# Kernel optimization log

Measured on AMD Instinct MI355X. Metric: run time of the kernel, lower is better.

## Reference

```python
import jax, jax.numpy as jnp
import numpy as np

MX_D, MN_D, CENTERS, WIDTH, SLOPE = 10.0, 0.0, 16, 1.0, 0.01
T_STEPS = 3


def _lrelu(x):
    return jax.nn.leaky_relu(x, SLOPE)


def _gauss(d):
    # d: [B,E,1] distances -> [B,E,CENTERS] gaussian radial basis
    mu = jnp.linspace(MN_D, MX_D, CENTERS, dtype=d.dtype)
    return jnp.exp(-jnp.square((d - mu[None, None, :]) / WIDTH))


def _equiv_message(v, idx2, n_recv, W1, W2, b, aw, ab):
    # v: [B,E,F] = concat(sender feats, receiver feats, bond feats).
    # Outer-product expand over receiver-cell axis (einsum with one-hot),
    # permutation-equivariant linear (local term + cell-sum term), LeakyReLU,
    # gather receiver cell, sigmoid attention gate, scatter_add to receivers.
    B, E, _ = v.shape
    O = W1.shape[1]
    oh = jax.nn.one_hot(idx2, n_recv, dtype=v.dtype)                 # [E,N]
    y_loc = jnp.einsum('bef,fo->beo', v, W1)                          # per-cell term
    y_sum = jnp.einsum('bef,fo->beo', v, W2) + b                      # cell-sum term (sum_n v*oh = v)
    y = _lrelu(y_loc[..., None] * oh[None, :, None, :] + y_sum[..., None])  # [B,E,O,N]
    gidx = jnp.broadcast_to(idx2[None, :, None, None], (B, E, O, 1))
    lat = jnp.take_along_axis(y, gidx, axis=3)[..., 0]                # [B,E,O]
    lat = jax.nn.sigmoid(lat @ aw + ab[None, None, :]) * lat          # attention gating
    return jnp.zeros((B, n_recv, O), v.dtype).at[:, idx2].add(lat)    # scatter_add over receivers


def _forward(sites, bonds, sites_p, bonds_sp, bonds_ps,
             se_W, se_b, sep_W, sep_b, ee_W, ee_b, eep_W, eep_b,
             eq_W1_ss, eq_W2_ss, eq_b_ss, att_w_ss, att_b_ss,
             eq_W1_ps, eq_W2_ps, eq_b_ps, att_w_ps, att_b_ps,
             eq_W1_sp, eq_W2_sp, eq_b_sp, att_w_sp, att_b_sp,
             nu_W1, nu_b1, nu_W2, nu_b2, nup_W1, nup_b1, nup_W2, nup_b2,
             p1_W, p1_b, p2a_W, p2a_b, p2b_W, p2b_b, p3_W, p3_b,
             idx1, idx2, idx1_sp, idx2_sp, idx1_ps, idx2_ps):
    s = _lrelu(sites @ se_W + se_b)          # [B,N,D] site embedding
    sp = _lrelu(sites_p @ sep_W + sep_b)     # [B,Np,D] pore embedding
    be = _lrelu(_gauss(bonds) @ ee_W + ee_b)
    bsp = _lrelu(_gauss(bonds_sp) @ eep_W + eep_b)
    bps = _lrelu(_gauss(bonds_ps) @ eep_W + eep_b)
    N, Np = s.shape[1], sp.shape[1]
    for t in range(T_STEPS):  # fixed number of message-passing layers
        v_ss = jnp.concatenate([s[:, idx1], s[:, idx2], be], -1)
        m = _equiv_message(v_ss, idx2, N, eq_W1_ss[t], eq_W2_ss[t], eq_b_ss[t], att_w_ss[t], att_b_ss[t])
        v_ps = jnp.concatenate([sp[:, idx1_ps], s[:, idx2_ps], bps], -1)
        m_ps = _equiv_message(v_ps, idx2_ps, N, eq_W1_ps[t], eq_W2_ps[t], eq_b_ps[t], att_w_ps[t], att_b_ps[t])
        v_sp = jnp.concatenate([s[:, idx1_sp], sp[:, idx2_sp], bsp], -1)
        m_sp = _equiv_message(v_sp, idx2_sp, Np, eq_W1_sp[t], eq_W2_sp[t], eq_b_sp[t], att_w_sp[t], att_b_sp[t])
        h = jnp.concatenate([s, m, m_ps], -1)
        h = _lrelu(_lrelu(h @ nu_W1[t] + nu_b1[t]) @ nu_W2[t] + nu_b2[t])
        s = s + h                              # residual node update (sites)
        hp = jnp.concatenate([sp, m_sp], -1)
        hp = _lrelu(_lrelu(hp @ nup_W1[t] + nup_b1[t]) @ nup_W2[t] + nup_b2[t])
        sp = sp + hp                           # residual node update (pores)
    x = _lrelu(s @ p1_W + p1_b).sum(1)        # sum pool over sites
    x = _lrelu(x @ p2a_W + p2a_b)
    x = _lrelu(x @ p2b_W + p2b_b)
    return x @ p3_W + p3_b                    # [B, out_size]


def setup_inputs():
    key = jax.random.key(0)
    ks = iter(jax.random.split(key, 80))
    B, N, Np, E, Esp = 4, 128, 16, 1280, 1024
    D, C, O, M, T = 32, CENTERS, 32, 64, T_STEPS
    Fin = 2 * D + 16  # sender + receiver + edge embedding

    def nrm(shape, fan):
        return jax.random.normal(next(ks), shape, jnp.float32) / np.float32(np.sqrt(fan))

    inp = {}
    inp['sites'] = jax.random.uniform(next(ks), (B, N, 1), jnp.float32)
    inp['bonds'] = jax.random.uniform(next(ks), (B, E, 1), jnp.float32) * MX_D
    inp['sites_p'] = jax.random.uniform(next(ks), (B, Np, 2), jnp.float32)
    inp['bonds_sp'] = jax.random.uniform(next(ks), (B, Esp, 1), jnp.float32) * MX_D
    inp['bonds_ps'] = jax.random.uniform(next(ks), (B, Esp, 1), jnp.float32) * MX_D
    inp['idx1'] = jax.random.randint(next(ks), (E,), 0, N, jnp.int32)
    inp['idx2'] = jax.random.randint(next(ks), (E,), 0, N, jnp.int32)
    inp['idx1_sp'] = jax.random.randint(next(ks), (Esp,), 0, N, jnp.int32)
    inp['idx2_sp'] = jax.random.randint(next(ks), (Esp,), 0, Np, jnp.int32)
    inp['idx1_ps'] = jax.random.randint(next(ks), (Esp,), 0, Np, jnp.int32)
    inp['idx2_ps'] = jax.random.randint(next(ks), (Esp,), 0, N, jnp.int32)
    # embeddings
    inp['se_W'] = nrm((1, D), 1); inp['se_b'] = nrm((D,), D)
    inp['sep_W'] = nrm((2, D), 2); inp['sep_b'] = nrm((D,), D)
    inp['ee_W'] = nrm((C, 16), C); inp['ee_b'] = nrm((16,), 16)
    inp['eep_W'] = nrm((C, 16), C); inp['eep_b'] = nrm((16,), 16)
    # equivariant message layers (stacked over T steps)
    for suf in ('ss', 'ps', 'sp'):
        inp['eq_W1_' + suf] = nrm((T, Fin, O), Fin)
        inp['eq_W2_' + suf] = nrm((T, Fin, O), Fin)
        inp['eq_b_' + suf] = nrm((T, O), O)
        inp['att_w_' + suf] = nrm((T, O, 1), O)
        inp['att_b_' + suf] = nrm((T, 1), 1)
    # node updates: sites take 2 message streams, pores take 1
    inp['nu_W1'] = nrm((T, D + 2 * O, D), D + 2 * O); inp['nu_b1'] = nrm((T, D), D)
    inp['nu_W2'] = nrm((T, D, D), D); inp['nu_b2'] = nrm((T, D), D)
    inp['nup_W1'] = nrm((T, D + O, D), D + O); inp['nup_b1'] = nrm((T, D), D)
    inp['nup_W2'] = nrm((T, D, D), D); inp['nup_b2'] = nrm((T, D), D)
    # prediction head
    inp['p1_W'] = nrm((D, M), D); inp['p1_b'] = nrm((M,), M)
    inp['p2a_W'] = nrm((M, M), M); inp['p2a_b'] = nrm((M,), M)
    inp['p2b_W'] = nrm((M, M), M); inp['p2b_b'] = nrm((M,), M)
    inp['p3_W'] = nrm((M, 1), M); inp['p3_b'] = nrm((1,), 1)
    return inp


def reference(sites, bonds, sites_p, bonds_sp, bonds_ps,
              se_W, se_b, sep_W, sep_b, ee_W, ee_b, eep_W, eep_b,
              eq_W1_ss, eq_W2_ss, eq_b_ss, att_w_ss, att_b_ss,
              eq_W1_ps, eq_W2_ps, eq_b_ps, att_w_ps, att_b_ps,
              eq_W1_sp, eq_W2_sp, eq_b_sp, att_w_sp, att_b_sp,
              nu_W1, nu_b1, nu_W2, nu_b2, nup_W1, nup_b1, nup_W2, nup_b2,
              p1_W, p1_b, p2a_W, p2a_b, p2b_W, p2b_b, p3_W, p3_b,
              idx1, idx2, idx1_sp, idx2_sp, idx1_ps, idx2_ps):
    return _forward(sites, bonds, sites_p, bonds_sp, bonds_ps,
                    se_W, se_b, sep_W, sep_b, ee_W, ee_b, eep_W, eep_b,
                    eq_W1_ss, eq_W2_ss, eq_b_ss, att_w_ss, att_b_ss,
                    eq_W1_ps, eq_W2_ps, eq_b_ps, att_w_ps, att_b_ps,
                    eq_W1_sp, eq_W2_sp, eq_b_sp, att_w_sp, att_b_sp,
                    nu_W1, nu_b1, nu_W2, nu_b2, nup_W1, nup_b1, nup_W2, nup_b2,
                    p1_W, p1_b, p2a_W, p2a_b, p2b_W, p2b_b, p3_W, p3_b,
                    idx1, idx2, idx1_sp, idx2_sp, idx1_ps, idx2_ps)
```

## Files before the change

kernel.cpp:

```cpp
#include <hip/hip_runtime.h>
#include <math.h>

#define BB   4
#define NN   128
#define NPP  16
#define EEE  1280
#define ESP  1024
#define DD   32
#define CC   16
#define OO   32
#define FIN  80
#define MMM  64
#define TT   3
#define TPB  256

constexpr int OFF_S    = 0;
constexpr int OFF_SP   = OFF_S    + BB*NN*DD;
constexpr int OFF_BE   = OFF_SP   + BB*NPP*DD;
constexpr int OFF_BSP  = OFF_BE   + BB*EEE*CC;
constexpr int OFF_BPS  = OFF_BSP  + BB*ESP*CC;
constexpr int OFF_MSS  = OFF_BPS  + BB*ESP*CC;
constexpr int OFF_MPS  = OFF_MSS  + TT*BB*NN*OO;
constexpr int OFF_MSP  = OFF_MPS  + TT*BB*NN*OO;
constexpr int OFF_MEND = OFF_MSP  + TT*BB*NPP*OO;
constexpr int ZM       = OFF_MEND - OFF_MSS;
constexpr int OFF_SASS = OFF_MEND;
constexpr int OFF_SBSS = OFF_SASS + BB*NN*OO;
constexpr int OFF_SBPS = OFF_SBSS + BB*NN*OO;
constexpr int OFF_SASP = OFF_SBPS + BB*NN*OO;
constexpr int OFF_PAPS = OFF_SASP + BB*NN*OO;
constexpr int OFF_PBSP = OFF_PAPS + BB*NPP*OO;
constexpr int WS_TOTAL = OFF_PBSP + BB*NPP*OO;

__device__ __forceinline__ float lrelu(float x) { return x > 0.f ? x : 0.01f * x; }

__device__ __forceinline__ void edge_embed(float d, const float* W, const float* bvec, float* out) {
    float g[CC];
#pragma unroll
    for (int c = 0; c < CC; ++c) {
        float mu = (10.0f / 15.0f) * (float)c;
        float z = d - mu;
        g[c] = expf(-z * z);
    }
#pragma unroll
    for (int j = 0; j < CC; ++j) {
        float a = bvec[j];
#pragma unroll
        for (int c = 0; c < CC; ++c) a += g[c] * W[c * CC + j];
        out[j] = lrelu(a);
    }
}

__global__ __launch_bounds__(TPB) void k_init(
    const float* sites, const float* bonds, const float* sites_p,
    const float* bonds_sp, const float* bonds_ps,
    const float* se_W, const float* se_b, const float* sep_W, const float* sep_b,
    const float* ee_W, const float* ee_b, const float* eep_W, const float* eep_b,
    const float* eqW1_ss, const float* eqW2_ss,
    const float* eqW1_ps, const float* eqW2_ps,
    const float* eqW1_sp, const float* eqW2_sp,
    float* ws)
{
    __shared__ float smem[4416];
    const int blk = blockIdx.x;
    const int tid = threadIdx.x;

    {
        const int totalA = ZM + BB*EEE + BB*ESP + BB*ESP;
        for (int i = blk*TPB + tid; i < totalA; i += gridDim.x*TPB) {
            int r = i;
            if (r < ZM) { ws[OFF_MSS + r] = 0.f; continue; }
            r -= ZM;
            if (r < BB*EEE) { edge_embed(bonds[r],    ee_W,  ee_b,  ws + OFF_BE  + r*CC); continue; }
            r -= BB*EEE;
            if (r < BB*ESP) { edge_embed(bonds_sp[r], eep_W, eep_b, ws + OFF_BSP + r*CC); continue; }
            r -= BB*ESP;
            edge_embed(bonds_ps[r], eep_W, eep_b, ws + OFF_BPS + r*CC);
        }
    }
    if (blk < 72) {
        const int el = tid >> 5, o = tid & 31;
        float* sP   = smem;
        float* sRow = smem + 4160;
        if (blk < 64) {
            const int g = blk*8 + el;
            float x = sites[g];
            float v0 = lrelu(x * se_W[o] + se_b[o]);
            ws[OFF_S + g*DD + o] = v0;
            sRow[el*32 + o] = v0;
            for (int i2 = tid; i2 < 4096; i2 += TPB) {
                int m = i2 >> 10, j = i2 & 1023, d = j >> 5, oo = j & 31;
                int row = (m == 1 || m == 2) ? (32 + d) : d;
                float wv;
                if (m < 2)      wv = eqW1_ss[row*OO + oo] + eqW2_ss[row*OO + oo];
                else if (m==2)  wv = eqW1_ps[row*OO + oo] + eqW2_ps[row*OO + oo];
                else            wv = eqW1_sp[row*OO + oo] + eqW2_sp[row*OO + oo];
                sP[i2] = wv;
            }
            __syncthreads();
            float p0=0.f,p1=0.f,p2=0.f,p3=0.f;
#pragma unroll
            for (int d = 0; d < 32; ++d) {
                float sv = sRow[el*32 + d];
                p0 += sv * sP[        d*32 + o];
                p1 += sv * sP[1024 +  d*32 + o];
                p2 += sv * sP[2048 +  d*32 + o];
                p3 += sv * sP[3072 +  d*32 + o];
            }
            ws[OFF_SASS + g*OO + o] = p0;
            ws[OFF_SBSS + g*OO + o] = p1;
            ws[OFF_SBPS + g*OO + o] = p2;
            ws[OFF_SASP + g*OO + o] = p3;
        } else {
            const int g = (blk-64)*8 + el;
            float x0 = sites_p[g*2], x1 = sites_p[g*2+1];
            float v0 = lrelu(x0 * sep_W[o] + x1 * sep_W[DD + o] + sep_b[o]);
            ws[OFF_SP + g*DD + o] = v0;
            sRow[el*32 + o] = v0;
            for (int i2 = tid; i2 < 2048; i2 += TPB) {
                int m = i2 >> 10, j = i2 & 1023, d = j >> 5, oo = j & 31;
                int row = (m == 0) ? d : (32 + d);
                float wv;
                if (m == 0) wv = eqW1_ps[row*OO + oo] + eqW2_ps[row*OO + oo];
                else        wv = eqW1_sp[row*OO + oo] + eqW2_sp[row*OO + oo];
                sP[i2] = wv;
            }
            __syncthreads();
            float p0=0.f,p1=0.f;
#pragma unroll
            for (int d = 0; d < 32; ++d) {
                float sv = sRow[el*32 + d];
                p0 += sv * sP[        d*32 + o];
                p1 += sv * sP[1024 +  d*32 + o];
            }
            ws[OFF_PAPS + g*OO + o] = p0;
            ws[OFF_PBSP + g*OO + o] = p1;
        }
    }
}

__global__ __launch_bounds__(TPB) void k_edges(
    const float* eqW1_ss, const float* eqW2_ss, const float* eqb_ss, const float* aw_ss, const float* ab_ss,
    const float* eqW1_ps, const float* eqW2_ps, const float* eqb_ps, const float* aw_ps, const float* ab_ps,
    const float* eqW1_sp, const float* eqW2_sp, const float* eqb_sp, const float* aw_sp, const float* ab_sp,
    const int* idx1, const int* idx2, const int* idx1_sp, const int* idx2_sp,
    const int* idx1_ps, const int* idx2_ps,
    float* ws, int t)
{
    __shared__ float sWe[CC*OO];
    __shared__ float sB[OO], sAw[OO];
    __shared__ float sAb;

    const int tid = threadIdx.x;
    const int blk = blockIdx.x;
    const int el = tid >> 5, o = tid & 31;

    constexpr int NB_SS = BB*EEE/8;
    constexpr int NB_PS = BB*ESP/8;

    const float *w1p, *w2p, *bp, *awp, *abp;
    const float *SAb, *SBb, *ef; float* mb;
    int s1, s2;

    if (blk < NB_SS) {
        const int rloc = blk*8 + el;
        const int b = rloc / EEE, e = rloc - b*EEE;
        s1 = idx1[e]; s2 = idx2[e];
        SAb = ws + OFF_SASS + b*(NN*OO);
        SBb = ws + OFF_SBSS + b*(NN*OO);
        ef  = ws + OFF_BE  + rloc*CC;
        mb  = ws + OFF_MSS + t*(BB*NN*OO) + b*(NN*OO);
        w1p = eqW1_ss; w2p = eqW2_ss; bp = eqb_ss; awp = aw_ss; abp = ab_ss;
    } else if (blk < NB_SS + NB_PS) {
        const int rloc = (blk - NB_SS)*8 + el;
        const int b = rloc >> 10, e = rloc & (ESP-1);
        s1 = idx1_ps[e]; s2 = idx2_ps[e];
        SAb = ws + OFF_PAPS + b*(NPP*OO);
        SBb = ws + OFF_SBPS + b*(NN*OO);
        ef  = ws + OFF_BPS + rloc*CC;
        mb  = ws + OFF_MPS + t*(BB*NN*OO) + b*(NN*OO);
        w1p = eqW1_ps; w2p = eqW2_ps; bp = eqb_ps; awp = aw_ps; abp = ab_ps;
    } else {
        const int rloc = (blk - NB_SS - NB_PS)*8 + el;
        const int b = rloc >> 10, e = rloc & (ESP-1);
        s1 = idx1_sp[e]; s2 = idx2_sp[e];
        SAb = ws + OFF_SASP + b*(NN*OO);
        SBb = ws + OFF_PBSP + b*(NPP*OO);
        ef  = ws + OFF_BSP + rloc*CC;
        mb  = ws + OFF_MSP + t*(BB*NPP*OO) + b*(NPP*OO);
        w1p = eqW1_sp; w2p = eqW2_sp; bp = eqb_sp; awp = aw_sp; abp = ab_sp;
    }

    const float* wa = w1p + t*(FIN*OO) + 2*DD*OO;
    const float* wb = w2p + t*(FIN*OO) + 2*DD*OO;
    for (int i = tid; i < CC*OO; i += TPB) sWe[i] = wa[i] + wb[i];
    if (tid < OO) { sB[tid] = bp[t*OO + tid]; sAw[tid] = awp[t*OO + tid]; }
    if (tid == 0) sAb = abp[t];
    __syncthreads();

    const float4 e0 = *(const float4*)(ef);
    const float4 e1 = *(const float4*)(ef + 4);
    const float4 e2 = *(const float4*)(ef + 8);
    const float4 e3 = *(const float4*)(ef + 12);

    float acc = sB[o] + SAb[s1*OO + o] + SBb[s2*OO + o];
    acc += e0.x*sWe[ 0*32+o] + e0.y*sWe[ 1*32+o] + e0.z*sWe[ 2*32+o] + e0.w*sWe[ 3*32+o];
    acc += e1.x*sWe[ 4*32+o] + e1.y*sWe[ 5*32+o] + e1.z*sWe[ 6*32+o] + e1.w*sWe[ 7*32+o];
    acc += e2.x*sWe[ 8*32+o] + e2.y*sWe[ 9*32+o] + e2.z*sWe[10*32+o] + e2.w*sWe[11*32+o];
    acc += e3.x*sWe[12*32+o] + e3.y*sWe[13*32+o] + e3.z*sWe[14*32+o] + e3.w*sWe[15*32+o];

    float u = lrelu(acc);
    float r = u * sAw[o];
#pragma unroll
    for (int mm = 16; mm > 0; mm >>= 1) r += __shfl_xor(r, mm, 32);
    float gate = 1.f / (1.f + expf(-(r + sAb)));
    atomicAdd(&mb[s2*OO + o], gate * u);
}

__global__ __launch_bounds__(TPB) void k_nodes(
    const float* nuW1, const float* nub1, const float* nuW2, const float* nub2,
    const float* nupW1, const float* nupb1, const float* nupW2, const float* nupb2,
    const float* eqW1_ss, const float* eqW2_ss,
    const float* eqW1_ps, const float* eqW2_ps,
    const float* eqW1_sp, const float* eqW2_sp,
    float* ws, int t)
{
    __shared__ float smem[5184];
    const int tid = threadIdx.x;
    const int blk = blockIdx.x;
    float* sW1 = smem;
    float* sW2 = smem + 3072;
    float* sb1 = smem + 4096;
    float* sb2 = smem + 4128;
    float* sh  = smem + 4160;
    float* su  = smem + 4928;
    const float* mss = ws + OFF_MSS + t*(BB*NN*OO);
    const float* mps = ws + OFF_MPS + t*(BB*NN*OO);
    const float* msp = ws + OFF_MSP + t*(BB*NPP*OO);
    const int el = tid >> 5, o = tid & 31;

    if (blk < 64) {
        const float* W1 = nuW1 + t*96*32;
        const float* W2 = nuW2 + t*32*32;
        for (int i = tid; i < 96*32; i += TPB) sW1[i] = W1[i];
        for (int i = tid; i < 32*32; i += TPB) sW2[i] = W2[i];
        if (tid < 32) { sb1[tid] = nub1[t*32 + tid]; sb2[tid] = nub2[t*32 + tid]; }
        for (int i = tid; i < 8*96; i += TPB) {
            int e2 = i / 96, f = i - e2*96;
            int g = blk*8 + e2;
            float v;
            if (f < 32)      v = ws[OFF_S + g*DD + f];
            else if (f < 64) v = mss[g*OO + (f-32)];
            else             v = mps[g*OO + (f-64)];
            sh[i] = v;
        }
        __syncthreads();
        float acc = sb1[o];
#pragma unroll
        for (int f = 0; f < 96; ++f) acc += sh[el*96 + f] * sW1[f*32 + o];
        su[el*32 + o] = lrelu(acc);
        __syncthreads();
        float acc2 = sb2[o];
#pragma unroll
        for (int k = 0; k < 32; ++k) acc2 += su[el*32 + k] * sW2[k*32 + o];
        const int g = blk*8 + el;
        float snew = sh[el*96 + o] + lrelu(acc2);
        __syncthreads();
        ws[OFF_S + g*DD + o] = snew;
        float* sRow = smem + 4928;
        sRow[el*32 + o] = snew;
        if (t < TT-1) {
            const int tn = t + 1;
            float* sP = smem;
            for (int i2 = tid; i2 < 4096; i2 += TPB) {
                int m = i2 >> 10, j = i2 & 1023, d = j >> 5, oo = j & 31;
                int row = (m == 1 || m == 2) ? (32 + d) : d;
                float wv;
                if (m < 2)     wv = eqW1_ss[tn*FIN*OO + row*OO + oo] + eqW2_ss[tn*FIN*OO + row*OO + oo];
                else if (m==2) wv = eqW1_ps[tn*FIN*OO + row*OO + oo] + eqW2_ps[tn*FIN*OO + row*OO + oo];
                else           wv = eqW1_sp[tn*FIN*OO + row*OO + oo] + eqW2_sp[tn*FIN*OO + row*OO + oo];
                sP[i2] = wv;
            }
            __syncthreads();
            float p0=0.f,p1=0.f,p2=0.f,p3=0.f;
#pragma unroll
            for (int d = 0; d < 32; ++d) {
                float sv = sRow[el*32 + d];
                p0 += sv * sP[        d*32 + o];
                p1 += sv * sP[1024 +  d*32 + o];
                p2 += sv * sP[2048 +  d*32 + o];
                p3 += sv * sP[3072 +  d*32 + o];
            }
            ws[OFF_SASS + g*OO + o] = p0;
            ws[OFF_SBSS + g*OO + o] = p1;
            ws[OFF_SBPS + g*OO + o] = p2;
            ws[OFF_SASP + g*OO + o] = p3;
        }
    } else {
        const int u2 = blk - 64;
        const float* W1 = nupW1 + t*64*32;
        const float* W2 = nupW2 + t*32*32;
        for (int i = tid; i < 64*32; i += TPB) sW1[i] = W1[i];
        for (int i = tid; i < 32*32; i += TPB) sW2[i] = W2[i];
        if (tid < 32) { sb1[tid] = nupb1[t*32 + tid]; sb2[tid] = nupb2[t*32 + tid]; }
        for (int i = tid; i < 8*64; i += TPB) {
            int e2 = i >> 6, f = i & 63;
            int g = u2*8 + e2;
            float v;
            if (f < 32) v = ws[OFF_SP + g*DD + f];
            else        v = msp[g*OO + (f-32)];
            sh[i] = v;
        }
        __syncthreads();
        float acc = sb1[o];
#pragma unroll
        for (int f = 0; f < 64; ++f) acc += sh[el*64 + f] * sW1[f*32 + o];
        su[el*32 + o] = lrelu(acc);
        __syncthreads();
        float acc2 = sb2[o];
#pragma unroll
        for (int k = 0; k < 32; ++k) acc2 += su[el*32 + k] * sW2[k*32 + o];
        const int g = u2*8 + el;
        float snew = sh[el*64 + o] + lrelu(acc2);
        __syncthreads();
        ws[OFF_SP + g*DD + o] = snew;
        float* sRow = smem + 4928;
        sRow[el*32 + o] = snew;
        if (t < TT-1) {
            const int tn = t + 1;
            float* sP = smem;
            for (int i2 = tid; i2 < 2048; i2 += TPB) {
                int m = i2 >> 10, j = i2 & 1023, d = j >> 5, oo = j & 31;
                int row = (m == 0) ? d : (32 + d);
                float wv;
                if (m == 0) wv = eqW1_ps[tn*FIN*OO + row*OO + oo] + eqW2_ps[tn*FIN*OO + row*OO + oo];
                else        wv = eqW1_sp[tn*FIN*OO + row*OO + oo] + eqW2_sp[tn*FIN*OO + row*OO + oo];
                sP[i2] = wv;
            }
            __syncthreads();
            float p0=0.f,p1=0.f;
#pragma unroll
            for (int d = 0; d < 32; ++d) {
                float sv = sRow[el*32 + d];
                p0 += sv * sP[        d*32 + o];
                p1 += sv * sP[1024 +  d*32 + o];
            }
            ws[OFF_PAPS + g*OO + o] = p0;
            ws[OFF_PBSP + g*OO + o] = p1;
        }
    }
}

__global__ __launch_bounds__(TPB) void k_head(
    const float* p1W, const float* p1b, const float* p2aW, const float* p2ab,
    const float* p2bW, const float* p2bb, const float* p3W, const float* p3b,
    const float* ws, float* out)
{
    __shared__ float sS[NN * DD];
    __shared__ float sW[DD * MMM];
    __shared__ float part[4][MMM];
    __shared__ float xv[MMM], yv[MMM], zv[MMM];

    const int b = blockIdx.x;
    const int tid = threadIdx.x;
    const float* s = ws + OFF_S + b * NN * DD;

    for (int i = tid; i < NN * DD; i += TPB) sS[i] = s[i];
    for (int i = tid; i < DD * MMM; i += TPB) sW[i] = p1W[i];
    __syncthreads();

    const int m = tid & 63;
    const int q = tid >> 6;
    float accp = 0.f;
    for (int n = q * 32; n < q * 32 + 32; ++n) {
        float a = p1b[m];
#pragma unroll
        for (int d = 0; d < DD; ++d) a += sS[n * DD + d] * sW[d * MMM + m];
        accp += lrelu(a);
    }
    part[q][m] = accp;
    __syncthreads();

    if (tid < MMM) xv[tid] = part[0][tid] + part[1][tid] + part[2][tid] + part[3][tid];
    __syncthreads();
    if (tid < MMM) {
        float a = p2ab[tid];
#pragma unroll
        for (int k = 0; k < MMM; ++k) a += xv[k] * p2aW[k * MMM + tid];
        yv[tid] = lrelu(a);
    }
    __syncthreads();
    if (tid < MMM) {
        float a = p2bb[tid];
#pragma unroll
        for (int k = 0; k < MMM; ++k) a += yv[k] * p2bW[k * MMM + tid];
        zv[tid] = lrelu(a);
    }
    __syncthreads();
    if (tid == 0) {
        float a = p3b[0];
#pragma unroll
        for (int k = 0; k < MMM; ++k) a += zv[k] * p3W[k];
        out[b] = a;
    }
}

extern "C" void kernel_launch(void* const* d_in, const int* in_sizes, int n_in,
                              void* d_out, int out_size, void* d_ws, size_t ws_size,
                              hipStream_t stream) {
    (void)in_sizes; (void)n_in; (void)out_size; (void)ws_size;
    const float* sites    = (const float*)d_in[0];
    const float* bonds    = (const float*)d_in[1];
    const float* sites_p  = (const float*)d_in[2];
    const float* bonds_sp = (const float*)d_in[3];
    const float* bonds_ps = (const float*)d_in[4];
    const int* idx1    = (const int*)d_in[5];
    const int* idx2    = (const int*)d_in[6];
    const int* idx1_sp = (const int*)d_in[7];
    const int* idx2_sp = (const int*)d_in[8];
    const int* idx1_ps = (const int*)d_in[9];
    const int* idx2_ps = (const int*)d_in[10];
    const float* se_W  = (const float*)d_in[11];
    const float* se_b  = (const float*)d_in[12];
    const float* sep_W = (const float*)d_in[13];
    const float* sep_b = (const float*)d_in[14];
    const float* ee_W  = (const float*)d_in[15];
    const float* ee_b  = (const float*)d_in[16];
    const float* eep_W = (const float*)d_in[17];
    const float* eep_b = (const float*)d_in[18];
    const float* eqW1_ss = (const float*)d_in[19];
    const float* eqW2_ss = (const float*)d_in[20];
    const float* eqb_ss  = (const float*)d_in[21];
    const float* aw_ss   = (const float*)d_in[22];
    const float* ab_ss   = (const float*)d_in[23];
    const float* eqW1_ps = (const float*)d_in[24];
    const float* eqW2_ps = (const float*)d_in[25];
    const float* eqb_ps  = (const float*)d_in[26];
    const float* aw_ps   = (const float*)d_in[27];
    const float* ab_ps   = (const float*)d_in[28];
    const float* eqW1_sp = (const float*)d_in[29];
    const float* eqW2_sp = (const float*)d_in[30];
    const float* eqb_sp  = (const float*)d_in[31];
    const float* aw_sp   = (const float*)d_in[32];
    const float* ab_sp   = (const float*)d_in[33];
    const float* nuW1  = (const float*)d_in[34];
    const float* nub1  = (const float*)d_in[35];
    const float* nuW2  = (const float*)d_in[36];
    const float* nub2  = (const float*)d_in[37];
    const float* nupW1 = (const float*)d_in[38];
    const float* nupb1 = (const float*)d_in[39];
    const float* nupW2 = (const float*)d_in[40];
    const float* nupb2 = (const float*)d_in[41];
    const float* p1W  = (const float*)d_in[42];
    const float* p1b  = (const float*)d_in[43];
    const float* p2aW = (const float*)d_in[44];
    const float* p2ab = (const float*)d_in[45];
    const float* p2bW = (const float*)d_in[46];
    const float* p2bb = (const float*)d_in[47];
    const float* p3W  = (const float*)d_in[48];
    const float* p3b  = (const float*)d_in[49];

    float* ws  = (float*)d_ws;
    float* out = (float*)d_out;

    k_init<<<256, TPB, 0, stream>>>(sites, bonds, sites_p, bonds_sp, bonds_ps,
                                    se_W, se_b, sep_W, sep_b, ee_W, ee_b, eep_W, eep_b,
                                    eqW1_ss, eqW2_ss, eqW1_ps, eqW2_ps, eqW1_sp, eqW2_sp, ws);

    const int edge_blocks = BB*EEE/8 + BB*ESP/8 + BB*ESP/8;
    for (int t = 0; t < TT; ++t) {
        k_edges<<<edge_blocks, TPB, 0, stream>>>(
            eqW1_ss, eqW2_ss, eqb_ss, aw_ss, ab_ss,
            eqW1_ps, eqW2_ps, eqb_ps, aw_ps, ab_ps,
            eqW1_sp, eqW2_sp, eqb_sp, aw_sp, ab_sp,
            idx1, idx2, idx1_sp, idx2_sp, idx1_ps, idx2_ps, ws, t);
        k_nodes<<<72, TPB, 0, stream>>>(nuW1, nub1, nuW2, nub2,
                                        nupW1, nupb1, nupW2, nupb2,
                                        eqW1_ss, eqW2_ss, eqW1_ps, eqW2_ps, eqW1_sp, eqW2_sp,
                                        ws, t);
    }
    k_head<<<4, TPB, 0, stream>>>(p1W, p1b, p2aW, p2ab, p2bW, p2bb, p3W, p3b, ws, out);
}
```

Measured before the change: 59.99 us.

## Fuse edge and node kernels via receiver CSR gather instead of atomics

Builds CSR lists of edges per receiver in the init kernel, then replaces the separate edge-scatter and node-update kernels with one per-step kernel. Each block gathers its receivers' incoming edges, reduces messages in shared memory, runs the node MLP and writes next-step projections. Projections are double-buffered so a single launch per step can read the old ones and write the new ones. The head's first layer pooling is folded in via atomics. This removes the atomic scatter and halves the launches per step, at the cost of serial CSR construction and less parallelism for high in-degree nodes.

Measured after the change: 196.1 us. 3.27x slower.

```diff
diff --git a/kernel.cpp b/kernel.cpp
--- a/kernel.cpp
+++ b/kernel.cpp
@@ -15,24 +15,45 @@
 #define TPB  256
 
 constexpr int OFF_S    = 0;
-constexpr int OFF_SP   = OFF_S    + BB*NN*DD;
-constexpr int OFF_BE   = OFF_SP   + BB*NPP*DD;
-constexpr int OFF_BSP  = OFF_BE   + BB*EEE*CC;
-constexpr int OFF_BPS  = OFF_BSP  + BB*ESP*CC;
-constexpr int OFF_MSS  = OFF_BPS  + BB*ESP*CC;
-constexpr int OFF_MPS  = OFF_MSS  + TT*BB*NN*OO;
-constexpr int OFF_MSP  = OFF_MPS  + TT*BB*NN*OO;
-constexpr int OFF_MEND = OFF_MSP  + TT*BB*NPP*OO;
-constexpr int ZM       = OFF_MEND - OFF_MSS;
-constexpr int OFF_SASS = OFF_MEND;
-constexpr int OFF_SBSS = OFF_SASS + BB*NN*OO;
-constexpr int OFF_SBPS = OFF_SBSS + BB*NN*OO;
-constexpr int OFF_SASP = OFF_SBPS + BB*NN*OO;
-constexpr int OFF_PAPS = OFF_SASP + BB*NN*OO;
-constexpr int OFF_PBSP = OFF_PAPS + BB*NPP*OO;
-constexpr int WS_TOTAL = OFF_PBSP + BB*NPP*OO;
+constexpr int OFF_SP   = OFF_S   + BB*NN*DD;
+constexpr int OFF_BE   = OFF_SP  + BB*NPP*DD;
+constexpr int OFF_BSP  = OFF_BE  + BB*EEE*CC;
+constexpr int OFF_BPS  = OFF_BSP + BB*ESP*CC;
+constexpr int OFF_PRJ  = OFF_BPS + BB*ESP*CC;
+constexpr int P_SASS = 0;
+constexpr int P_SBSS = P_SASS + BB*NN*OO;
+constexpr int P_SBPS = P_SBSS + BB*NN*OO;
+constexpr int P_SASP = P_SBPS + BB*NN*OO;
+constexpr int P_PAPS = P_SASP + BB*NN*OO;
+constexpr int P_PBSP = P_PAPS + BB*NPP*OO;
+constexpr int PRJ_SZ = P_PBSP + BB*NPP*OO;
+constexpr int OFF_POOL = OFF_PRJ + 2*PRJ_SZ;
+constexpr int OFF_CSR  = OFF_POOL + BB*MMM;
+constexpr int SS_PTR  = 0;
+constexpr int SS_LIST = SS_PTR + NN + 1;
+constexpr int PS_PTR  = SS_LIST + EEE;
+constexpr int PS_LIST = PS_PTR + NN + 1;
+constexpr int SP_PTR  = PS_LIST + ESP;
+constexpr int SP_LIST = SP_PTR + NPP + 1;
 
 __device__ __forceinline__ float lrelu(float x) { return x > 0.f ? x : 0.01f * x; }
+
+__device__ __forceinline__ float dot16(const float* ef, const float* sWe, int o) {
+    float4 f0 = *(const float4*)(ef);
+    float4 f1 = *(const float4*)(ef + 4);
+    float4 f2 = *(const float4*)(ef + 8);
+    float4 f3 = *(const float4*)(ef + 12);
+    return f0.x*sWe[ 0*32+o] + f0.y*sWe[ 1*32+o] + f0.z*sWe[ 2*32+o] + f0.w*sWe[ 3*32+o]
+         + f1.x*sWe[ 4*32+o] + f1.y*sWe[ 5*32+o] + f1.z*sWe[ 6*32+o] + f1.w*sWe[ 7*32+o]
+         + f2.x*sWe[ 8*32+o] + f2.y*sWe[ 9*32+o] + f2.z*sWe[10*32+o] + f2.w*sWe[11*32+o]
+         + f3.x*sWe[12*32+o] + f3.y*sWe[13*32+o] + f3.z*sWe[14*32+o] + f3.w*sWe[15*32+o];
+}
+
+__device__ __forceinline__ float red32(float r) {
+#pragma unroll
+    for (int mm = 16; mm > 0; mm >>= 1) r += __shfl_xor(r, mm, 32);
+    return r;
+}
 
 __device__ __forceinline__ void edge_embed(float d, const float* W, const float* bvec, float* out) {
     float g[CC];
@@ -51,9 +72,30 @@
     }
 }
 
+__device__ void csr_build(const int* recv, int E, int R, int* ptr, int* list, int* scnt) {
+    const int tid = threadIdx.x;
+    if (tid < R) {
+        int c = 0;
+        for (int e = 0; e < E; ++e) c += (recv[e] == tid) ? 1 : 0;
+        scnt[tid] = c;
+    }
+    __syncthreads();
+    if (tid == 0) {
+        int run = 0;
+        for (int i = 0; i < R; ++i) { int c = scnt[i]; scnt[i] = run; ptr[i] = run; run += c; }
+        ptr[R] = run;
+    }
+    __syncthreads();
+    if (tid < R) {
+        int pos = scnt[tid];
+        for (int e = 0; e < E; ++e) if (recv[e] == tid) list[pos++] = e;
+    }
+}
+
 __global__ __launch_bounds__(TPB) void k_init(
     const float* sites, const float* bonds, const float* sites_p,
     const float* bonds_sp, const float* bonds_ps,
+    const int* idx2, const int* idx2_ps, const int* idx2_sp,
     const float* se_W, const float* se_b, const float* sep_W, const float* sep_b,
     const float* ee_W, const float* ee_b, const float* eep_W, const float* eep_b,
     const float* eqW1_ss, const float* eqW2_ss,
@@ -66,11 +108,11 @@
     const int tid = threadIdx.x;
 
     {
-        const int totalA = ZM + BB*EEE + BB*ESP + BB*ESP;
+        const int totalA = BB*MMM + BB*EEE + BB*ESP + BB*ESP;
         for (int i = blk*TPB + tid; i < totalA; i += gridDim.x*TPB) {
             int r = i;
-            if (r < ZM) { ws[OFF_MSS + r] = 0.f; continue; }
-            r -= ZM;
+            if (r < BB*MMM) { ws[OFF_POOL + r] = 0.f; continue; }
+            r -= BB*MMM;
             if (r < BB*EEE) { edge_embed(bonds[r],    ee_W,  ee_b,  ws + OFF_BE  + r*CC); continue; }
             r -= BB*EEE;
             if (r < BB*ESP) { edge_embed(bonds_sp[r], eep_W, eep_b, ws + OFF_BSP + r*CC); continue; }
@@ -79,6 +121,7 @@
         }
     }
     if (blk < 72) {
+        float* prj0 = ws + OFF_PRJ;
         const int el = tid >> 5, o = tid & 31;
         float* sP   = smem;
         float* sRow = smem + 4160;
@@ -90,7 +133,7 @@
             sRow[el*32 + o] = v0;
             for (int i2 = tid; i2 < 4096; i2 += TPB) {
                 int m = i2 >> 10, j = i2 & 1023, d = j >> 5, oo = j & 31;
-                int row = (m == 1 || m == 2) ? (32 + d) : d;
+                int row = (m == 1 || m == 2) ? (DD + d) : d;
                 float wv;
                 if (m < 2)      wv = eqW1_ss[row*OO + oo] + eqW2_ss[row*OO + oo];
                 else if (m==2)  wv = eqW1_ps[row*OO + oo] + eqW2_ps[row*OO + oo];
@@ -107,10 +150,10 @@
                 p2 += sv * sP[2048 +  d*32 + o];
                 p3 += sv * sP[3072 +  d*32 + o];
             }
-            ws[OFF_SASS + g*OO + o] = p0;
-            ws[OFF_SBSS + g*OO + o] = p1;
-            ws[OFF_SBPS + g*OO + o] = p2;
-            ws[OFF_SASP + g*OO + o] = p3;
+            prj0[P_SASS + g*OO + o] = p0;
+            prj0[P_SBSS + g*OO + o] = p1;
+            prj0[P_SBPS + g*OO + o] = p2;
+            prj0[P_SASP + g*OO + o] = p3;
         } else {
             const int g = (blk-64)*8 + el;
             float x0 = sites_p[g*2], x1 = sites_p[g*2+1];
@@ -119,7 +162,7 @@
             sRow[el*32 + o] = v0;
             for (int i2 = tid; i2 < 2048; i2 += TPB) {
                 int m = i2 >> 10, j = i2 & 1023, d = j >> 5, oo = j & 31;
-                int row = (m == 0) ? d : (32 + d);
+                int row = (m == 0) ? d : (DD + d);
                 float wv;
                 if (m == 0) wv = eqW1_ps[row*OO + oo] + eqW2_ps[row*OO + oo];
                 else        wv = eqW1_sp[row*OO + oo] + eqW2_sp[row*OO + oo];
@@ -133,275 +176,214 @@
                 p0 += sv * sP[        d*32 + o];
                 p1 += sv * sP[1024 +  d*32 + o];
             }
-            ws[OFF_PAPS + g*OO + o] = p0;
-            ws[OFF_PBSP + g*OO + o] = p1;
-        }
-    }
-}
-
-__global__ __launch_bounds__(TPB) void k_edges(
+            prj0[P_PAPS + g*OO + o] = p0;
+            prj0[P_PBSP + g*OO + o] = p1;
+        }
+    }
+    if (blk >= 253) {
+        int* csr  = (int*)(ws + OFF_CSR);
+        int* scnt = (int*)smem;
+        if (blk == 255)      csr_build(idx2,    EEE, NN,  csr + SS_PTR, csr + SS_LIST, scnt);
+        else if (blk == 254) csr_build(idx2_ps, ESP, NN,  csr + PS_PTR, csr + PS_LIST, scnt);
+        else                 csr_build(idx2_sp, ESP, NPP, csr + SP_PTR, csr + SP_LIST, scnt);
+    }
+}
+
+__global__ __launch_bounds__(TPB) void k_step(
     const float* eqW1_ss, const float* eqW2_ss, const float* eqb_ss, const float* aw_ss, const float* ab_ss,
     const float* eqW1_ps, const float* eqW2_ps, const float* eqb_ps, const float* aw_ps, const float* ab_ps,
     const float* eqW1_sp, const float* eqW2_sp, const float* eqb_sp, const float* aw_sp, const float* ab_sp,
-    const int* idx1, const int* idx2, const int* idx1_sp, const int* idx2_sp,
-    const int* idx1_ps, const int* idx2_ps,
+    const int* idx1, const int* idx1_ps, const int* idx1_sp,
+    const float* nuW1, const float* nub1, const float* nuW2, const float* nub2,
+    const float* nupW1, const float* nupb1, const float* nupW2, const float* nupb2,
+    const float* p1W, const float* p1b,
     float* ws, int t)
 {
-    __shared__ float sWe[CC*OO];
-    __shared__ float sB[OO], sAw[OO];
-    __shared__ float sAb;
-
-    const int tid = threadIdx.x;
-    const int blk = blockIdx.x;
-    const int el = tid >> 5, o = tid & 31;
-
-    constexpr int NB_SS = BB*EEE/8;
-    constexpr int NB_PS = BB*ESP/8;
-
-    const float *w1p, *w2p, *bp, *awp, *abp;
-    const float *SAb, *SBb, *ef; float* mb;
-    int s1, s2;
-
-    if (blk < NB_SS) {
-        const int rloc = blk*8 + el;
-        const int b = rloc / EEE, e = rloc - b*EEE;
-        s1 = idx1[e]; s2 = idx2[e];
-        SAb = ws + OFF_SASS + b*(NN*OO);
-        SBb = ws + OFF_SBSS + b*(NN*OO);
-        ef  = ws + OFF_BE  + rloc*CC;
-        mb  = ws + OFF_MSS + t*(BB*NN*OO) + b*(NN*OO);
-        w1p = eqW1_ss; w2p = eqW2_ss; bp = eqb_ss; awp = aw_ss; abp = ab_ss;
-    } else if (blk < NB_SS + NB_PS) {
-        const int rloc = (blk - NB_SS)*8 + el;
-        const int b = rloc >> 10, e = rloc & (ESP-1);
-        s1 = idx1_ps[e]; s2 = idx2_ps[e];
-        SAb = ws + OFF_PAPS + b*(NPP*OO);
-        SBb = ws + OFF_SBPS + b*(NN*OO);
-        ef  = ws + OFF_BPS + rloc*CC;
-        mb  = ws + OFF_MPS + t*(BB*NN*OO) + b*(NN*OO);
-        w1p = eqW1_ps; w2p = eqW2_ps; bp = eqb_ps; awp = aw_ps; abp = ab_ps;
-    } else {
-        const int rloc = (blk - NB_SS - NB_PS)*8 + el;
-        const int b = rloc >> 10, e = rloc & (ESP-1);
-        s1 = idx1_sp[e]; s2 = idx2_sp[e];
-        SAb = ws + OFF_SASP + b*(NN*OO);
-        SBb = ws + OFF_PBSP + b*(NPP*OO);
-        ef  = ws + OFF_BSP + rloc*CC;
-        mb  = ws + OFF_MSP + t*(BB*NPP*OO) + b*(NPP*OO);
-        w1p = eqW1_sp; w2p = eqW2_sp; bp = eqb_sp; awp = aw_sp; abp = ab_sp;
-    }
-
-    const float* wa = w1p + t*(FIN*OO) + 2*DD*OO;
-    const float* wb = w2p + t*(FIN*OO) + 2*DD*OO;
-    for (int i = tid; i < CC*OO; i += TPB) sWe[i] = wa[i] + wb[i];
-    if (tid < OO) { sB[tid] = bp[t*OO + tid]; sAw[tid] = awp[t*OO + tid]; }
-    if (tid == 0) sAb = abp[t];
-    __syncthreads();
-
-    const float4 e0 = *(const float4*)(ef);
-    const float4 e1 = *(const float4*)(ef + 4);
-    const float4 e2 = *(const float4*)(ef + 8);
-    const float4 e3 = *(const float4*)(ef + 12);
-
-    float acc = sB[o] + SAb[s1*OO + o] + SBb[s2*OO + o];
-    acc += e0.x*sWe[ 0*32+o] + e0.y*sWe[ 1*32+o] + e0.z*sWe[ 2*32+o] + e0.w*sWe[ 3*32+o];
-    acc += e1.x*sWe[ 4*32+o] + e1.y*sWe[ 5*32+o] + e1.z*sWe[ 6*32+o] + e1.w*sWe[ 7*32+o];
-    acc += e2.x*sWe[ 8*32+o] + e2.y*sWe[ 9*32+o] + e2.z*sWe[10*32+o] + e2.w*sWe[11*32+o];
-    acc += e3.x*sWe[12*32+o] + e3.y*sWe[13*32+o] + e3.z*sWe[14*32+o] + e3.w*sWe[15*32+o];
-
-    float u = lrelu(acc);
-    float r = u * sAw[o];
-#pragma unroll
-    for (int mm = 16; mm > 0; mm >>= 1) r += __shfl_xor(r, mm, 32);
-    float gate = 1.f / (1.f + expf(-(r + sAb)));
-    atomicAdd(&mb[s2*OO + o], gate * u);
-}
-
-__global__ __launch_bounds__(TPB) void k_nodes(
-    const float* nuW1, const float* nub1, const float* nuW2, const float* nub2,
-    const float* nupW1, const float* nupb1, const float* nupW2, const float* nupb2,
-    const float* eqW1_ss, const float* eqW2_ss,
-    const float* eqW1_ps, const float* eqW2_ps,
-    const float* eqW1_sp, const float* eqW2_sp,
-    float* ws, int t)
-{
-    __shared__ float smem[5184];
-    const int tid = threadIdx.x;
-    const int blk = blockIdx.x;
-    float* sW1 = smem;
-    float* sW2 = smem + 3072;
-    float* sb1 = smem + 4096;
-    float* sb2 = smem + 4128;
-    float* sh  = smem + 4160;
-    float* su  = smem + 4928;
-    const float* mss = ws + OFF_MSS + t*(BB*NN*OO);
-    const float* mps = ws + OFF_MPS + t*(BB*NN*OO);
-    const float* msp = ws + OFF_MSP + t*(BB*NPP*OO);
-    const int el = tid >> 5, o = tid & 31;
-
-    if (blk < 64) {
-        const float* W1 = nuW1 + t*96*32;
-        const float* W2 = nuW2 + t*32*32;
-        for (int i = tid; i < 96*32; i += TPB) sW1[i] = W1[i];
-        for (int i = tid; i < 32*32; i += TPB) sW2[i] = W2[i];
-        if (tid < 32) { sb1[tid] = nub1[t*32 + tid]; sb2[tid] = nub2[t*32 + tid]; }
-        for (int i = tid; i < 8*96; i += TPB) {
-            int e2 = i / 96, f = i - e2*96;
-            int g = blk*8 + e2;
-            float v;
-            if (f < 32)      v = ws[OFF_S + g*DD + f];
-            else if (f < 64) v = mss[g*OO + (f-32)];
-            else             v = mps[g*OO + (f-64)];
-            sh[i] = v;
-        }
-        __syncthreads();
-        float acc = sb1[o];
-#pragma unroll
-        for (int f = 0; f < 96; ++f) acc += sh[el*96 + f] * sW1[f*32 + o];
-        su[el*32 + o] = lrelu(acc);
-        __syncthreads();
-        float acc2 = sb2[o];
-#pragma unroll
-        for (int k = 0; k < 32; ++k) acc2 += su[el*32 + k] * sW2[k*32 + o];
-        const int g = blk*8 + el;
-        float snew = sh[el*96 + o] + lrelu(acc2);
-        __syncthreads();
-        ws[OFF_S + g*DD + o] = snew;
-        float* sRow = smem + 4928;
-        sRow[el*32 + o] = snew;
+    __shared__ float sWe1[512], sWe2[512], sRed[512], sH[192], sU[64], sSnew[64];
+    const int tid = threadIdx.x, blk = blockIdx.x;
+    const int slot = tid >> 5, o = tid & 31;
+    const int par = t & 1;
+    const float* PRJ  = ws + OFF_PRJ + par * PRJ_SZ;
+    float*       PRJn = ws + OFF_PRJ + (par ^ 1) * PRJ_SZ;
+    const int* csr = (const int*)(ws + OFF_CSR);
+
+    if (blk < 256) {
+        const int r = slot >> 2, q = slot & 3;
+        for (int i = tid; i < 512; i += TPB) {
+            sWe1[i] = eqW1_ss[t*FIN*OO + 2*DD*OO + i] + eqW2_ss[t*FIN*OO + 2*DD*OO + i];
+            sWe2[i] = eqW1_ps[t*FIN*OO + 2*DD*OO + i] + eqW2_ps[t*FIN*OO + 2*DD*OO + i];
+        }
+        __syncthreads();
+        const int g = blk*2 + r, b = g >> 7, n = g & 127;
+        const float bias_ss = eqb_ss[t*OO+o], awo_ss = aw_ss[t*OO+o], abs_ss = ab_ss[t];
+        const float bias_ps = eqb_ps[t*OO+o], awo_ps = aw_ps[t*OO+o], abs_ps = ab_ps[t];
+        const float sb_ss = PRJ[P_SBSS + g*OO + o];
+        const float sb_ps = PRJ[P_SBPS + g*OO + o];
+        const float* SAss = PRJ + P_SASS + b*(NN*OO);
+        const float* PAps = PRJ + P_PAPS + b*(NPP*OO);
+        const float* BEb  = ws + OFF_BE  + b*(EEE*CC);
+        const float* BPSb = ws + OFF_BPS + b*(ESP*CC);
+        float acc_ss = 0.f, acc_ps = 0.f;
+        {
+            const int e0 = csr[SS_PTR + n], e1 = csr[SS_PTR + n + 1];
+            for (int k = e0 + q; k < e1; k += 4) {
+                const int e = csr[SS_LIST + k];
+                const int s1 = idx1[e];
+                float a = bias_ss + sb_ss + SAss[s1*OO + o] + dot16(BEb + e*CC, sWe1, o);
+                float u = lrelu(a);
+                float rr = red32(u * awo_ss);
+                acc_ss += u / (1.f + expf(-(rr + abs_ss)));
+            }
+        }
+        {
+            const int e0 = csr[PS_PTR + n], e1 = csr[PS_PTR + n + 1];
+            for (int k = e0 + q; k < e1; k += 4) {
+                const int e = csr[PS_LIST + k];
+                const int s1 = idx1_ps[e];
+                float a = bias_ps + sb_ps + PAps[s1*OO + o] + dot16(BPSb + e*CC, sWe2, o);
+                float u = lrelu(a);
+                float rr = red32(u * awo_ps);
+                acc_ps += u / (1.f + expf(-(rr + abs_ps)));
+            }
+        }
+        sRed[slot*64 + o]      = acc_ss;
+        sRed[slot*64 + 32 + o] = acc_ps;
+        if (tid < 64) sH[(tid>>5)*96 + (tid&31)] = ws[OFF_S + (blk*2 + (tid>>5))*DD + (tid&31)];
+        __syncthreads();
+        if (tid < 128) {
+            const int r2 = tid >> 6, c = tid & 63;
+            sH[r2*96 + 32 + c] = sRed[(r2*4  )*64 + c] + sRed[(r2*4+1)*64 + c]
+                               + sRed[(r2*4+2)*64 + c] + sRed[(r2*4+3)*64 + c];
+        }
+        __syncthreads();
+        if (tid < 64) {
+            const int r2 = tid >> 5, oo = tid & 31;
+            const float* W1 = nuW1 + t*(96*32);
+            float a = nub1[t*32 + oo];
+#pragma unroll
+            for (int f = 0; f < 96; ++f) a += sH[r2*96 + f] * W1[f*32 + oo];
+            sU[r2*32 + oo] = lrelu(a);
+        }
+        __syncthreads();
+        if (tid < 64) {
+            const int r2 = tid >> 5, oo = tid & 31;
+            const float* W2 = nuW2 + t*(32*32);
+            float a = nub2[t*32 + oo];
+#pragma unroll
+            for (int k2 = 0; k2 < 32; ++k2) a += sU[r2*32 + k2] * W2[k2*32 + oo];
+            const float snew = sH[r2*96 + oo] + lrelu(a);
+            ws[OFF_S + (blk*2 + r2)*DD + oo] = snew;
+            sSnew[r2*32 + oo] = snew;
+        }
+        __syncthreads();
         if (t < TT-1) {
             const int tn = t + 1;
-            float* sP = smem;
-            for (int i2 = tid; i2 < 4096; i2 += TPB) {
-                int m = i2 >> 10, j = i2 & 1023, d = j >> 5, oo = j & 31;
-                int row = (m == 1 || m == 2) ? (32 + d) : d;
-                float wv;
-                if (m < 2)     wv = eqW1_ss[tn*FIN*OO + row*OO + oo] + eqW2_ss[tn*FIN*OO + row*OO + oo];
-                else if (m==2) wv = eqW1_ps[tn*FIN*OO + row*OO + oo] + eqW2_ps[tn*FIN*OO + row*OO + oo];
-                else           wv = eqW1_sp[tn*FIN*OO + row*OO + oo] + eqW2_sp[tn*FIN*OO + row*OO + oo];
-                sP[i2] = wv;
-            }
-            __syncthreads();
-            float p0=0.f,p1=0.f,p2=0.f,p3=0.f;
-#pragma unroll
-            for (int d = 0; d < 32; ++d) {
-                float sv = sRow[el*32 + d];
-                p0 += sv * sP[        d*32 + o];
-                p1 += sv * sP[1024 +  d*32 + o];
-                p2 += sv * sP[2048 +  d*32 + o];
-                p3 += sv * sP[3072 +  d*32 + o];
-            }
-            ws[OFF_SASS + g*OO + o] = p0;
-            ws[OFF_SBSS + g*OO + o] = p1;
-            ws[OFF_SBPS + g*OO + o] = p2;
-            ws[OFF_SASP + g*OO + o] = p3;
+            const int r2 = slot >> 2, m = slot & 3;
+            const int g2 = blk*2 + r2;
+            const float *w1m, *w2m; float* dst;
+            if (m == 0)      { w1m = eqW1_ss + tn*FIN*OO;         w2m = eqW2_ss + tn*FIN*OO;         dst = PRJn + P_SASS; }
+            else if (m == 1) { w1m = eqW1_ss + tn*FIN*OO + DD*OO; w2m = eqW2_ss + tn*FIN*OO + DD*OO; dst = PRJn + P_SBSS; }
+            else if (m == 2) { w1m = eqW1_ps + tn*FIN*OO + DD*OO; w2m = eqW2_ps + tn*FIN*OO + DD*OO; dst = PRJn + P_SBPS; }
+            else             { w1m = eqW1_sp + tn*FIN*OO;         w2m = eqW2_sp + tn*FIN*OO;         dst = PRJn + P_SASP; }
+            float a = 0.f;
+#pragma unroll
+            for (int d = 0; d < 32; ++d) a += sSnew[r2*32 + d] * (w1m[d*OO + o] + w2m[d*OO + o]);
+            dst[g2*OO + o] = a;
+        } else if (tid < 128) {
+            const int r2 = tid >> 6, mm = tid & 63;
+            const int g2 = blk*2 + r2, b2 = g2 >> 7;
+            float a = p1b[mm];
+#pragma unroll
+            for (int d = 0; d < 32; ++d) a += sSnew[r2*32 + d] * p1W[d*MMM + mm];
+            atomicAdd(&ws[OFF_POOL + b2*MMM + mm], lrelu(a));
         }
     } else {
-        const int u2 = blk - 64;
-        const float* W1 = nupW1 + t*64*32;
-        const float* W2 = nupW2 + t*32*32;
-        for (int i = tid; i < 64*32; i += TPB) sW1[i] = W1[i];
-        for (int i = tid; i < 32*32; i += TPB) sW2[i] = W2[i];
-        if (tid < 32) { sb1[tid] = nupb1[t*32 + tid]; sb2[tid] = nupb2[t*32 + tid]; }
-        for (int i = tid; i < 8*64; i += TPB) {
-            int e2 = i >> 6, f = i & 63;
-            int g = u2*8 + e2;
-            float v;
-            if (f < 32) v = ws[OFF_SP + g*DD + f];
-            else        v = msp[g*OO + (f-32)];
-            sh[i] = v;
-        }
-        __syncthreads();
-        float acc = sb1[o];
-#pragma unroll
-        for (int f = 0; f < 64; ++f) acc += sh[el*64 + f] * sW1[f*32 + o];
-        su[el*32 + o] = lrelu(acc);
-        __syncthreads();
-        float acc2 = sb2[o];
-#pragma unroll
-        for (int k = 0; k < 32; ++k) acc2 += su[el*32 + k] * sW2[k*32 + o];
-        const int g = u2*8 + el;
-        float snew = sh[el*64 + o] + lrelu(acc2);
-        __syncthreads();
-        ws[OFF_SP + g*DD + o] = snew;
-        float* sRow = smem + 4928;
-        sRow[el*32 + o] = snew;
-        if (t < TT-1) {
+        for (int i = tid; i < 512; i += TPB)
+            sWe1[i] = eqW1_sp[t*FIN*OO + 2*DD*OO + i] + eqW2_sp[t*FIN*OO + 2*DD*OO + i];
+        __syncthreads();
+        const int g = blk - 256, b = g >> 4, p = g & 15;
+        const float bias_sp = eqb_sp[t*OO+o], awo_sp = aw_sp[t*OO+o], abs_sp = ab_sp[t];
+        const float sb_sp = PRJ[P_PBSP + g*OO + o];
+        const float* SAsp = PRJ + P_SASP + b*(NN*OO);
+        const float* BSPb = ws + OFF_BSP + b*(ESP*CC);
+        float acc_sp = 0.f;
+        {
+            const int e0 = csr[SP_PTR + p], e1 = csr[SP_PTR + p + 1];
+            for (int k = e0 + slot; k < e1; k += 8) {
+                const int e = csr[SP_LIST + k];
+                const int s1 = idx1_sp[e];
+                float a = bias_sp + sb_sp + SAsp[s1*OO + o] + dot16(BSPb + e*CC, sWe1, o);
+                float u = lrelu(a);
+                float rr = red32(u * awo_sp);
+                acc_sp += u / (1.f + expf(-(rr + abs_sp)));
+            }
+        }
+        sRed[slot*32 + o] = acc_sp;
+        if (tid < 32) sH[tid] = ws[OFF_SP + g*DD + tid];
+        __syncthreads();
+        if (tid < 32) {
+            float mv = 0.f;
+#pragma unroll
+            for (int s2 = 0; s2 < 8; ++s2) mv += sRed[s2*32 + tid];
+            sH[32 + tid] = mv;
+        }
+        __syncthreads();
+        if (tid < 32) {
+            const float* W1 = nupW1 + t*(64*32);
+            float a = nupb1[t*32 + tid];
+#pragma unroll
+            for (int f = 0; f < 64; ++f) a += sH[f] * W1[f*32 + tid];
+            sU[tid] = lrelu(a);
+        }
+        __syncthreads();
+        if (tid < 32) {
+            const float* W2 = nupW2 + t*(32*32);
+            float a = nupb2[t*32 + tid];
+#pragma unroll
+            for (int k2 = 0; k2 < 32; ++k2) a += sU[k2] * W2[k2*32 + tid];
+            const float snew = sH[tid] + lrelu(a);
+            ws[OFF_SP + g*DD + tid] = snew;
+            sSnew[tid] = snew;
+        }
+        __syncthreads();
+        if (t < TT-1 && tid < 64) {
             const int tn = t + 1;
-            float* sP = smem;
-            for (int i2 = tid; i2 < 2048; i2 += TPB) {
-                int m = i2 >> 10, j = i2 & 1023, d = j >> 5, oo = j & 31;
-                int row = (m == 0) ? d : (32 + d);
-                float wv;
-                if (m == 0) wv = eqW1_ps[tn*FIN*OO + row*OO + oo] + eqW2_ps[tn*FIN*OO + row*OO + oo];
-                else        wv = eqW1_sp[tn*FIN*OO + row*OO + oo] + eqW2_sp[tn*FIN*OO + row*OO + oo];
-                sP[i2] = wv;
-            }
-            __syncthreads();
-            float p0=0.f,p1=0.f;
-#pragma unroll
-            for (int d = 0; d < 32; ++d) {
-                float sv = sRow[el*32 + d];
-                p0 += sv * sP[        d*32 + o];
-                p1 += sv * sP[1024 +  d*32 + o];
-            }
-            ws[OFF_PAPS + g*OO + o] = p0;
-            ws[OFF_PBSP + g*OO + o] = p1;
+            const int m = tid >> 5, oo = tid & 31;
+            const float *w1m, *w2m; float* dst;
+            if (m == 0) { w1m = eqW1_ps + tn*FIN*OO;         w2m = eqW2_ps + tn*FIN*OO;         dst = PRJn + P_PAPS; }
+            else        { w1m = eqW1_sp + tn*FIN*OO + DD*OO; w2m = eqW2_sp + tn*FIN*OO + DD*OO; dst = PRJn + P_PBSP; }
+            float a = 0.f;
+#pragma unroll
+            for (int d = 0; d < 32; ++d) a += sSnew[d] * (w1m[d*OO + oo] + w2m[d*OO + oo]);
+            dst[g*OO + oo] = a;
         }
     }
 }
 
 __global__ __launch_bounds__(TPB) void k_head(
-    const float* p1W, const float* p1b, const float* p2aW, const float* p2ab,
-    const float* p2bW, const float* p2bb, const float* p3W, const float* p3b,
-    const float* ws, float* out)
+    const float* p2aW, const float* p2ab, const float* p2bW, const float* p2bb,
+    const float* p3W, const float* p3b, const float* ws, float* out)
 {
-    __shared__ float sS[NN * DD];
-    __shared__ float sW[DD * MMM];
-    __shared__ float part[4][MMM];
-    __shared__ float xv[MMM], yv[MMM], zv[MMM];
-
-    const int b = blockIdx.x;
+    __shared__ float sx[256], sy[256], sz[256];
     const int tid = threadIdx.x;
-    const float* s = ws + OFF_S + b * NN * DD;
-
-    for (int i = tid; i < NN * DD; i += TPB) sS[i] = s[i];
-    for (int i = tid; i < DD * MMM; i += TPB) sW[i] = p1W[i];
+    sx[tid] = ws[OFF_POOL + tid];
     __syncthreads();
-
-    const int m = tid & 63;
-    const int q = tid >> 6;
-    float accp = 0.f;
-    for (int n = q * 32; n < q * 32 + 32; ++n) {
-        float a = p1b[m];
-#pragma unroll
-        for (int d = 0; d < DD; ++d) a += sS[n * DD + d] * sW[d * MMM + m];
-        accp += lrelu(a);
-    }
-    part[q][m] = accp;
+    const int b = tid >> 6, mm = tid & 63;
+    float a = p2ab[mm];
+#pragma unroll
+    for (int k = 0; k < MMM; ++k) a += sx[b*64 + k] * p2aW[k*MMM + mm];
+    sy[tid] = lrelu(a);
     __syncthreads();
-
-    if (tid < MMM) xv[tid] = part[0][tid] + part[1][tid] + part[2][tid] + part[3][tid];
+    a = p2bb[mm];
+#pragma unroll
+    for (int k = 0; k < MMM; ++k) a += sy[b*64 + k] * p2bW[k*MMM + mm];
+    sz[tid] = lrelu(a);
     __syncthreads();
-    if (tid < MMM) {
-        float a = p2ab[tid];
-#pragma unroll
-        for (int k = 0; k < MMM; ++k) a += xv[k] * p2aW[k * MMM + tid];
-        yv[tid] = lrelu(a);
-    }
-    __syncthreads();
-    if (tid < MMM) {
-        float a = p2bb[tid];
-#pragma unroll
-        for (int k = 0; k < MMM; ++k) a += yv[k] * p2bW[k * MMM + tid];
-        zv[tid] = lrelu(a);
-    }
-    __syncthreads();
-    if (tid == 0) {
-        float a = p3b[0];
-#pragma unroll
-        for (int k = 0; k < MMM; ++k) a += zv[k] * p3W[k];
-        out[b] = a;
+    if (tid < BB) {
+        float acc = p3b[0];
+#pragma unroll
+        for (int k = 0; k < MMM; ++k) acc += sz[tid*64 + k] * p3W[k];
+        out[tid] = acc;
     }
 }
 
@@ -464,20 +446,17 @@
     float* out = (float*)d_out;
 
     k_init<<<256, TPB, 0, stream>>>(sites, bonds, sites_p, bonds_sp, bonds_ps,
+                                    idx2, idx2_ps, idx2_sp,
                                     se_W, se_b, sep_W, sep_b, ee_W, ee_b, eep_W, eep_b,
                                     eqW1_ss, eqW2_ss, eqW1_ps, eqW2_ps, eqW1_sp, eqW2_sp, ws);
-
-    const int edge_blocks = BB*EEE/8 + BB*ESP/8 + BB*ESP/8;
     for (int t = 0; t < TT; ++t) {
-        k_edges<<<edge_blocks, TPB, 0, stream>>>(
+        k_step<<<320, TPB, 0, stream>>>(
             eqW1_ss, eqW2_ss, eqb_ss, aw_ss, ab_ss,
             eqW1_ps, eqW2_ps, eqb_ps, aw_ps, ab_ps,
             eqW1_sp, eqW2_sp, eqb_sp, aw_sp, ab_sp,
-            idx1, idx2, idx1_sp, idx2_sp, idx1_ps, idx2_ps, ws, t);
-        k_nodes<<<72, TPB, 0, stream>>>(nuW1, nub1, nuW2, nub2,
-                                        nupW1, nupb1, nupW2, nupb2,
-                                        eqW1_ss, eqW2_ss, eqW1_ps, eqW2_ps, eqW1_sp, eqW2_sp,
-                                        ws, t);
-    }
-    k_head<<<4, TPB, 0, stream>>>(p1W, p1b, p2aW, p2ab, p2bW, p2bb, p3W, p3b, ws, out);
-}
+            idx1, idx1_ps, idx1_sp,
+            nuW1, nub1, nuW2, nub2, nupW1, nupb1, nupW2, nupb2,
+            p1W, p1b, ws, t);
+    }
+    k_head<<<1, TPB, 0, stream>>>(p2aW, p2ab, p2bW, p2bb, p3W, p3b, ws, out);
+}
```
